# Performance work log

Measured on AMD Instinct MI355X. Metric: run time of the kernel, lower is better.

The kernel has to match this reference:

```python
import jax, jax.numpy as jnp
import numpy as np

K = 40  # neighbors, self.k = 40 in the module
BN_EPS = 1e-5


def knn(x, k):
    # x: (B, C, N) -> indices of k nearest points (largest negative sq-dist)
    xx = jnp.sum(x * x, axis=1, keepdims=True)            # (B, 1, N)
    inner = -2.0 * jnp.einsum('bcn,bcm->bnm', x, x)       # (B, N, N)
    pd = -xx - inner - jnp.swapaxes(xx, 1, 2)             # (B, N, N) = -||xi-xj||^2
    _, idx = jax.lax.top_k(pd, k)                         # (B, N, k)
    return idx


def graph_cov(x, k):
    # Faithful port of get_graph_dynamic_covariance (dim9=False, idx=None)
    B, C, N = x.shape
    idx = knn(x, k)                                       # (B, N, k)
    xt = jnp.swapaxes(x, 1, 2)                            # (B, N, C)
    feature = xt[jnp.arange(B)[:, None, None], idx]       # gather: (B, N, k, C)
    xc = xt[:, :, None, :]                                # (B, N, 1, C)
    rel = feature - xc                                    # relative positions
    var = jnp.var(rel, axis=2, ddof=1)                    # torch.var is unbiased
    relf = rel * (1.0 - var)[:, :, None, :]
    relf = jnp.concatenate([jnp.broadcast_to(xc, rel.shape), relf], axis=3)
    norm = rel - jnp.mean(rel, axis=0)                    # mean over BATCH dim, as in source
    cov = jnp.einsum('bnkc,bnjc->bnkj', rel, norm)        # (B, N, k, k)
    out = jnp.concatenate([relf, cov], axis=3)            # (B, N, k, 2C+k)
    return jnp.transpose(out, (0, 3, 1, 2))               # (B, 2C+k, N, k)


def bn(x, g, b):
    # train-mode BatchNorm (batch statistics, biased variance), eps=1e-5
    axes = (0,) + tuple(range(2, x.ndim))
    m = jnp.mean(x, axis=axes, keepdims=True)
    v = jnp.var(x, axis=axes, keepdims=True)
    shp = (1, -1) + (1,) * (x.ndim - 2)
    return g.reshape(shp) * (x - m) * jax.lax.rsqrt(v + BN_EPS) + b.reshape(shp)


def blk(x, W, g, b):
    # Conv(1x1, no bias) + BN + LeakyReLU(0.2)
    return jax.nn.leaky_relu(bn(jnp.einsum('oi,bi...->bo...', W, x), g, b), 0.2)


def forward(x, l, W3, W4, W5, W6, W7, W8, W9, W10, W11, W12,
            g3, b3, g4, b4, g5, b5, g6, b6, g7, b7, g8, b8, g9, b9,
            g10, b10, g11, b11):
    B, _, N = x.shape
    rc = blk(blk(graph_cov(x, K), W3, g3, b3), W4, g4, b4)       # (B,64,N,K)
    rc_ = jnp.max(rc, axis=-1)                                    # (B,64,N)
    drc = blk(blk(graph_cov(rc_, K), W5, g5, b5), W6, g6, b6)
    drc_ = jnp.max(drc, axis=-1)                                  # (B,64,N)
    allf = jnp.concatenate([rc_, drc_], axis=1)                   # (B,128,N)
    h = jnp.max(blk(allf, W7, g7, b7), axis=-1, keepdims=True)    # (B,1024,1)
    lv = blk(l.reshape(B, -1, 1), W8, g8, b8)                     # (B,64,1)
    h = jnp.concatenate([h, lv], axis=1)                          # (B,1088,1)
    h = jnp.broadcast_to(h, (B, h.shape[1], N))
    h = jnp.concatenate([h, rc_, drc_], axis=1)                   # (B,1216,N)
    h = blk(h, W9, g9, b9)
    h = blk(h, W10, g10, b10)                                     # dropout is eval-mode identity
    h = blk(h, W11, g11, b11)
    return jnp.einsum('oi,bin->bon', W12, h)                      # (B,50,N)


def setup_inputs():
    key = jax.random.key(0)
    ks = jax.random.split(key, 12)
    B, N = 4, 2048
    d = {}
    d['x'] = jax.random.normal(ks[0], (B, 3, N), jnp.float32)
    lab = jax.random.randint(ks[1], (B,), 0, 16)
    d['l'] = jax.nn.one_hot(lab, 16, dtype=jnp.float32)
    wdims = {'W3': (64, 46), 'W4': (64, 64), 'W5': (64, 168), 'W6': (64, 64),
             'W7': (1024, 128), 'W8': (64, 16), 'W9': (512, 1216),
             'W10': (256, 512), 'W11': (128, 256), 'W12': (50, 128)}
    for i, (name, shp) in enumerate(wdims.items()):
        d[name] = jax.random.normal(ks[2 + i], shp, jnp.float32) / np.float32(np.sqrt(shp[1]))
    for name, c in [('g3', 64), ('g4', 64), ('g5', 64), ('g6', 64), ('g7', 1024),
                    ('g8', 64), ('g9', 512), ('g10', 256), ('g11', 128)]:
        d[name] = jnp.ones((c,), jnp.float32)
        d['b' + name[1:]] = jnp.zeros((c,), jnp.float32)
    return d


def reference(x, l, W3, W4, W5, W6, W7, W8, W9, W10, W11, W12,
              g3, b3, g4, b4, g5, b5, g6, b6, g7, b7, g8, b8, g9, b9,
              g10, b10, g11, b11):
    return forward(x, l, W3, W4, W5, W6, W7, W8, W9, W10, W11, W12,
                   g3, b3, g4, b4, g5, b5, g6, b6, g7, b7, g8, b8, g9, b9,
                   g10, b10, g11, b11)
```

## Files before the change

kernel.cpp:

```cpp
#include <hip/hip_runtime.h>
#include <math.h>

#define NB 4
#define NP 2048
#define KNN 40
#define BEPS 1e-5f
#define NSLOT 64
#define CMCH 16

typedef unsigned long long u64;

static __device__ __forceinline__ float leaky(float x) { return x >= 0.f ? x : 0.2f * x; }

static __device__ __forceinline__ u64 keyOf(float v, int m) {
  unsigned u = __float_as_uint(v);
  u ^= (u >> 31) ? 0xFFFFFFFFu : 0x80000000u;
  return ((u64)u << 32) | (unsigned)(NP - 1 - m);
}
static __device__ __forceinline__ u64 umax64(u64 a, u64 b) { return a > b ? a : b; }

__global__ __launch_bounds__(256) void canary_kernel(float* __restrict__ out, int n, float val) {
  int i = blockIdx.x*256 + threadIdx.x;
  if (i < n) out[i] = val;
}

__global__ __launch_bounds__(256) void knn3_kernel(const float* __restrict__ x, int* __restrict__ idx) {
  int b = blockIdx.y, n = blockIdx.x, tid = threadIdx.x;
  __shared__ float pd[NP];
  __shared__ u64 red[256];
  __shared__ u64 red2[32];
  __shared__ int sh_w;
  float xn0 = x[(b*3+0)*NP+n], xn1 = x[(b*3+1)*NP+n], xn2 = x[(b*3+2)*NP+n];
  float xxn = __fadd_rn(__fadd_rn(__fmul_rn(xn0,xn0), __fmul_rn(xn1,xn1)), __fmul_rn(xn2,xn2));
  for (int m = tid; m < NP; m += 256) {
    float m0 = x[(b*3+0)*NP+m], m1 = x[(b*3+1)*NP+m], m2 = x[(b*3+2)*NP+m];
    float xxm = __fadd_rn(__fadd_rn(__fmul_rn(m0,m0), __fmul_rn(m1,m1)), __fmul_rn(m2,m2));
    float dot = __fmaf_rn(xn2, m2, __fmaf_rn(xn1, m1, __fmul_rn(xn0, m0)));
    float inner = __fmul_rn(-2.f, dot);
    pd[m] = __fsub_rn(__fsub_rn(-xxm, inner), xxn);
  }
  __syncthreads();
  u64 myBest = 0;
  #pragma unroll
  for (int j = 0; j < 8; ++j) myBest = umax64(myBest, keyOf(pd[tid + j*256], tid + j*256));
  for (int kk = 0; kk < KNN; ++kk) {
    red[tid] = myBest;
    __syncthreads();
    if (tid < 32) {
      u64 h = red[tid];
      #pragma unroll
      for (int j = 1; j < 8; ++j) h = umax64(h, red[tid + j*32]);
      red2[tid] = h;
    }
    __syncthreads();
    if (tid == 0) {
      u64 h = red2[0];
      #pragma unroll
      for (int j = 1; j < 32; ++j) h = umax64(h, red2[j]);
      int w = NP - 1 - (int)(h & 0xFFFFFFFFu);
      idx[(b*NP+n)*KNN + kk] = w;
      pd[w] = -INFINITY;
      sh_w = w;
    }
    __syncthreads();
    if ((sh_w & 255) == tid) {
      u64 nb = 0;
      #pragma unroll
      for (int j = 0; j < 8; ++j) nb = umax64(nb, keyOf(pd[tid + j*256], tid + j*256));
      myBest = nb;
    }
  }
}

__global__ __launch_bounds__(256) void xx64_kernel(const float* __restrict__ rc, float* __restrict__ xx) {
  int i = blockIdx.x*256 + threadIdx.x;
  if (i >= NB*NP) return;
  const float* p = &rc[(size_t)i*64];
  float s = __fmul_rn(p[0], p[0]);
  #pragma unroll
  for (int c = 1; c < 64; ++c) s = __fadd_rn(s, __fmul_rn(p[c], p[c]));
  xx[i] = s;
}

__global__ __launch_bounds__(256) void knn64_kernel(const float* __restrict__ rc, const float* __restrict__ xx,
                                                    int* __restrict__ idx) {
  int b = blockIdx.y, n = blockIdx.x, tid = threadIdx.x;
  __shared__ float pd[NP];
  __shared__ float xn[64];
  __shared__ u64 red[256];
  __shared__ u64 red2[32];
  __shared__ int sh_w;
  if (tid < 64) xn[tid] = rc[((size_t)b*NP+n)*64 + tid];
  __syncthreads();
  float xxn = xx[b*NP+n];
  for (int m = tid; m < NP; m += 256) {
    const float* xm = &rc[((size_t)b*NP+m)*64];
    float dot = __fmul_rn(xn[0], xm[0]);
    #pragma unroll
    for (int c = 1; c < 64; ++c) dot = __fmaf_rn(xn[c], xm[c], dot);
    float inner = __fmul_rn(-2.f, dot);
    pd[m] = __fsub_rn(__fsub_rn(-xx[b*NP+m], inner), xxn);
  }
  __syncthreads();
  u64 myBest = 0;
  #pragma unroll
  for (int j = 0; j < 8; ++j) myBest = umax64(myBest, keyOf(pd[tid + j*256], tid + j*256));
  for (int kk = 0; kk < KNN; ++kk) {
    red[tid] = myBest;
    __syncthreads();
    if (tid < 32) {
      u64 h = red[tid];
      #pragma unroll
      for (int j = 1; j < 8; ++j) h = umax64(h, red[tid + j*32]);
      red2[tid] = h;
    }
    __syncthreads();
    if (tid == 0) {
      u64 h = red2[0];
      #pragma unroll
      for (int j = 1; j < 32; ++j) h = umax64(h, red2[j]);
      int w = NP - 1 - (int)(h & 0xFFFFFFFFu);
      idx[(b*NP+n)*KNN + kk] = w;
      pd[w] = -INFINITY;
      sh_w = w;
    }
    __syncthreads();
    if ((sh_w & 255) == tid) {
      u64 nb = 0;
      #pragma unroll
      for (int j = 0; j < 8; ++j) nb = umax64(nb, keyOf(pd[tid + j*256], tid + j*256));
      myBest = nb;
    }
  }
}


__global__ __launch_bounds__(256) void s1a_kernel(
    const float* __restrict__ x, const int* __restrict__ idx1, const float* __restrict__ W3,
    double* __restrict__ stslots, float* __restrict__ y)
{
  int b = blockIdx.y, n = blockIdx.x, tid = threadIdx.x;
  __shared__ int sidx[4][KNN];
  __shared__ float rs[KNN][4];
  __shared__ float ns[KNN][4];
  __shared__ float scale[3];
  __shared__ __align__(16) float feat[KNN*48];
  __shared__ float w3s[64*48];
  __shared__ double sred[4][64];

  for (int i = tid; i < 4*KNN; i += 256) sidx[i/KNN][i%KNN] = idx1[((i/KNN)*NP + n)*KNN + (i%KNN)];
  for (int i = tid; i < 64*48; i += 256) { int o = i/48, ci = i%48; w3s[i] = (ci < 46) ? W3[o*46+ci] : 0.f; }
  __syncthreads();
  for (int i = tid; i < KNN*3; i += 256) {
    int k = i/3, c = i%3;
    float ctr = x[(b*3+c)*NP + n];
    float r = x[(b*3+c)*NP + sidx[b][k]] - ctr;
    float s = 0.f;
    for (int b2 = 0; b2 < 4; ++b2) s += x[(b2*3+c)*NP + sidx[b2][k]] - x[(b2*3+c)*NP + n];
    rs[k][c] = r; ns[k][c] = r - 0.25f*s;
  }
  __syncthreads();
  if (tid < 3) {
    float s = 0.f; for (int k = 0; k < KNN; ++k) s += rs[k][tid];
    float m = s/(float)KNN; float v = 0.f;
    for (int k = 0; k < KNN; ++k) { float d = rs[k][tid]-m; v += d*d; }
    scale[tid] = 1.f - v/(float)(KNN-1);
  }
  __syncthreads();
  for (int i = tid; i < KNN*48; i += 256) {
    int k = i/48, ci = i%48; float v;
    if (ci < 3) v = x[(b*3+ci)*NP+n];
    else if (ci < 6) v = rs[k][ci-3]*scale[ci-3];
    else if (ci < 46) { int j = ci-6; v = rs[k][0]*ns[j][0] + rs[k][1]*ns[j][1] + rs[k][2]*ns[j][2]; }
    else v = 0.f;
    feat[i] = v;
  }
  __syncthreads();

  int o = tid & 63, kg = tid >> 6;
  float acc[10];
  #pragma unroll
  for (int t = 0; t < 10; ++t) acc[t] = 0.f;
  for (int ci4 = 0; ci4 < 12; ++ci4) {
    float w0 = w3s[o*48+ci4*4+0], w1 = w3s[o*48+ci4*4+1], w2 = w3s[o*48+ci4*4+2], w3c = w3s[o*48+ci4*4+3];
    #pragma unroll
    for (int t = 0; t < 10; ++t) {
      float4 f4 = *(const float4*)&feat[(kg*10+t)*48 + ci4*4];
      acc[t] += f4.x*w0 + f4.y*w1 + f4.z*w2 + f4.w*w3c;
    }
  }
  size_t bn40 = (size_t)(b*NP+n)*KNN;
  #pragma unroll
  for (int t = 0; t < 10; ++t) y[(bn40 + kg*10+t)*64 + o] = acc[t];
  double s = 0.0, s2 = 0.0;
  #pragma unroll
  for (int t = 0; t < 10; ++t) { double a = acc[t]; s += a; s2 += a*a; }
  int slot = (blockIdx.y*NP + blockIdx.x) & (NSLOT-1);
  sred[kg][o] = s; __syncthreads();
  if (kg == 0) atomicAdd(&stslots[slot*128 + o], sred[0][o]+sred[1][o]+sred[2][o]+sred[3][o]);
  __syncthreads();
  sred[kg][o] = s2; __syncthreads();
  if (kg == 0) atomicAdd(&stslots[slot*128 + 64 + o], sred[0][o]+sred[1][o]+sred[2][o]+sred[3][o]);
}

__global__ __launch_bounds__(256) void s2a_kernel(
    const float* __restrict__ rc, const int* __restrict__ idx2, const float* __restrict__ W5,
    double* __restrict__ stslots, float* __restrict__ y)
{
  int b = blockIdx.y, n = blockIdx.x, tid = threadIdx.x;
  __shared__ int sidx[4][KNN];
  __shared__ float rsT[64*41];
  __shared__ float nsT[64*41];
  __shared__ float scale[64];
  __shared__ __align__(16) float feat[KNN*168];
  __shared__ double sred[4][64];

  for (int i = tid; i < 4*KNN; i += 256) sidx[i/KNN][i%KNN] = idx2[((i/KNN)*NP + n)*KNN + (i%KNN)];
  __syncthreads();
  for (int i = tid; i < KNN*64; i += 256) {
    int k = i >> 6, c = i & 63;
    float ctr = rc[((size_t)(b*NP+n))*64 + c];
    float r = rc[((size_t)(b*NP) + sidx[b][k])*64 + c] - ctr;
    float s = 0.f;
    for (int b2 = 0; b2 < 4; ++b2)
      s += rc[((size_t)(b2*NP) + sidx[b2][k])*64 + c] - rc[((size_t)(b2*NP+n))*64 + c];
    rsT[c*41+k] = r; nsT[c*41+k] = r - 0.25f*s;
  }
  __syncthreads();
  if (tid < 64) {
    int c = tid;
    float s = 0.f; for (int k = 0; k < KNN; ++k) s += rsT[c*41+k];
    float m = s/(float)KNN; float v = 0.f;
    for (int k = 0; k < KNN; ++k) { float d = rsT[c*41+k]-m; v += d*d; }
    scale[c] = 1.f - v/(float)(KNN-1);
  }
  __syncthreads();
  for (int i = tid; i < KNN*128; i += 256) {
    int k = i >> 7, ci = i & 127;
    float v;
    if (ci < 64) v = rc[((size_t)(b*NP+n))*64 + ci];
    else v = rsT[(ci-64)*41 + k]*scale[ci-64];
    feat[k*168 + ci] = v;
  }
  for (int p = tid; p < KNN*KNN; p += 256) {
    int k = p/KNN, j = p%KNN;
    float acc = __fmul_rn(rsT[k], nsT[j]);
    #pragma unroll 8
    for (int c = 1; c < 64; ++c) acc = __fmaf_rn(rsT[c*41+k], nsT[c*41+j], acc);
    feat[k*168 + 128 + j] = acc;
  }
  __syncthreads();

  int o = tid & 63, kg = tid >> 6;
  float acc[10];
  #pragma unroll
  for (int t = 0; t < 10; ++t) acc[t] = 0.f;
  for (int ci4 = 0; ci4 < 42; ++ci4) {
    float4 wv = *(const float4*)&W5[(size_t)o*168 + ci4*4];
    #pragma unroll
    for (int t = 0; t < 10; ++t) {
      float4 f4 = *(const float4*)&feat[(kg*10+t)*168 + ci4*4];
      acc[t] += f4.x*wv.x + f4.y*wv.y + f4.z*wv.z + f4.w*wv.w;
    }
  }
  size_t bn40 = (size_t)(b*NP+n)*KNN;
  #pragma unroll
  for (int t = 0; t < 10; ++t) y[(bn40 + kg*10+t)*64 + o] = acc[t];
  double s = 0.0, s2 = 0.0;
  #pragma unroll
  for (int t = 0; t < 10; ++t) { double a = acc[t]; s += a; s2 += a*a; }
  int slot = (blockIdx.y*NP + blockIdx.x) & (NSLOT-1);
  sred[kg][o] = s; __syncthreads();
  if (kg == 0) atomicAdd(&stslots[slot*128 + o], sred[0][o]+sred[1][o]+sred[2][o]+sred[3][o]);
  __syncthreads();
  sred[kg][o] = s2; __syncthreads();
  if (kg == 0) atomicAdd(&stslots[slot*128 + 64 + o], sred[0][o]+sred[1][o]+sred[2][o]+sred[3][o]);
}

__global__ __launch_bounds__(256) void mid_kernel(
    float* __restrict__ y, const float* __restrict__ W,
    const double* __restrict__ stp, const float* __restrict__ gv, const float* __restrict__ bv,
    double* __restrict__ stslots)
{
  int b = blockIdx.y, n = blockIdx.x, tid = threadIdx.x;
  __shared__ float m_s[64], sc_s[64], bo_s[64];
  __shared__ __align__(16) float ytile[KNN*68];
  __shared__ double sred[4][64];
  const double INV_M1 = 1.0/327680.0;

  if (tid < 64) {
    double md = stp[tid]*INV_M1;
    double vd = stp[64+tid]*INV_M1 - md*md;
    m_s[tid] = (float)md;
    sc_s[tid] = gv[tid]/sqrtf((float)vd + BEPS);
    bo_s[tid] = bv[tid];
  }
  __syncthreads();
  size_t bn40 = (size_t)(b*NP+n)*KNN;
  for (int i = tid; i < KNN*64; i += 256) {
    int k = i >> 6, c = i & 63;
    float v = y[(bn40 + k)*64 + c];
    ytile[k*68+c] = leaky(sc_s[c]*(v - m_s[c]) + bo_s[c]);
  }
  __syncthreads();
  int o = tid & 63, kg = tid >> 6;
  float acc2[10];
  #pragma unroll
  for (int t = 0; t < 10; ++t) acc2[t] = 0.f;
  for (int c4 = 0; c4 < 16; ++c4) {
    float4 wv = *(const float4*)&W[(size_t)o*64 + c4*4];
    #pragma unroll
    for (int t = 0; t < 10; ++t) {
      float4 y4 = *(const float4*)&ytile[(kg*10+t)*68 + c4*4];
      acc2[t] += y4.x*wv.x + y4.y*wv.y + y4.z*wv.z + y4.w*wv.w;
    }
  }
  #pragma unroll
  for (int t = 0; t < 10; ++t) y[(bn40 + kg*10+t)*64 + o] = acc2[t];
  double s = 0.0, s2 = 0.0;
  #pragma unroll
  for (int t = 0; t < 10; ++t) { double a = acc2[t]; s += a; s2 += a*a; }
  int slot = (blockIdx.y*NP + blockIdx.x) & (NSLOT-1);
  sred[kg][o] = s; __syncthreads();
  if (kg == 0) atomicAdd(&stslots[slot*128 + o], sred[0][o]+sred[1][o]+sred[2][o]+sred[3][o]);
  __syncthreads();
  sred[kg][o] = s2; __syncthreads();
  if (kg == 0) atomicAdd(&stslots[slot*128 + 64 + o], sred[0][o]+sred[1][o]+sred[2][o]+sred[3][o]);
}

__global__ __launch_bounds__(256) void maxk_bn_kernel(
    const float* __restrict__ y, const double* __restrict__ stp,
    const float* __restrict__ gv, const float* __restrict__ bv, float* __restrict__ out)
{
  int i = blockIdx.x*256 + threadIdx.x;
  if (i >= NB*NP*64) return;
  int o = i & 63; int bn = i >> 6;
  const double INV_M1 = 1.0/327680.0;
  double md = stp[o]*INV_M1;
  double vd = stp[64+o]*INV_M1 - md*md;
  float m = (float)md;
  float sc = gv[o]/sqrtf((float)vd + BEPS);
  float bo = bv[o];
  float mx = -INFINITY;
  size_t base = (size_t)bn*KNN;
  for (int k = 0; k < KNN; ++k) {
    float v = y[(base + k)*64 + o];
    mx = fmaxf(mx, leaky(sc*(v-m) + bo));
  }
  out[(size_t)bn*64 + o] = mx;
}

__global__ __launch_bounds__(128) void redstats_kernel(const double* __restrict__ slots, double* __restrict__ st) {
  int c = threadIdx.x;
  double s = 0.0;
  for (int i = 0; i < NSLOT; ++i) s += slots[i*128 + c];
  st[c] = s;
}

__global__ __launch_bounds__(256) void allf_kernel(const float* __restrict__ rc, const float* __restrict__ drc,
                                                   float* __restrict__ out) {
  int i = blockIdx.x*256 + threadIdx.x;
  if (i >= NB*NP*128) return;
  int c = i & 127; int bn = i >> 7;
  out[i] = (c < 64) ? rc[(size_t)bn*64 + c] : drc[(size_t)bn*64 + (c-64)];
}

#define GBM 64
#define GBN 64
#define GBK 16
__global__ __launch_bounds__(256) void gemm_kernel(const float* __restrict__ A, const float* __restrict__ W,
                                                   float* __restrict__ C, int M, int No, int Kd,
                                                   int wstride, int woff, const float* __restrict__ bias) {
  __shared__ __align__(16) float As[GBK][GBM+8];
  __shared__ __align__(16) float Ws[GBK][GBN+8];
  int bm = blockIdx.y * GBM, bn = blockIdx.x * GBN;
  int tid = threadIdx.x;
  int tx = tid % 16, ty = tid / 16;
  float acc[4][4] = {{0.f}};
  for (int k0 = 0; k0 < Kd; k0 += GBK) {
    for (int i = tid; i < GBM*GBK; i += 256) {
      int r = i / GBK, c = i % GBK;
      int gm = bm + r, gk = k0 + c;
      As[c][r] = (gk < Kd && gm < M) ? A[(size_t)gm*Kd + gk] : 0.f;
      int gn = bn + r;
      Ws[c][r] = (gk < Kd && gn < No) ? W[(size_t)gn*wstride + woff + gk] : 0.f;
    }
    __syncthreads();
    #pragma unroll
    for (int kk = 0; kk < GBK; ++kk) {
      float4 a4 = *(const float4*)&As[kk][ty*4];
      float4 w4 = *(const float4*)&Ws[kk][tx*4];
      float av[4] = {a4.x, a4.y, a4.z, a4.w};
      float wv[4] = {w4.x, w4.y, w4.z, w4.w};
      #pragma unroll
      for (int i2 = 0; i2 < 4; ++i2)
        #pragma unroll
        for (int j2 = 0; j2 < 4; ++j2)
          acc[i2][j2] += av[i2]*wv[j2];
    }
    __syncthreads();
  }
  for (int i2 = 0; i2 < 4; ++i2) {
    int gm = bm + ty*4 + i2;
    if (gm >= M) continue;
    for (int j2 = 0; j2 < 4; ++j2) {
      int gn = bn + tx*4 + j2;
      if (gn < No) {
        float v = acc[i2][j2];
        if (bias) v += bias[(gm >> 11)*No + gn];
        C[(size_t)gm*No + gn] = v;
      }
    }
  }
}

__global__ __launch_bounds__(256) void colstats_kernel(const float* __restrict__ A, long M, int C,
                                                       int rowsPerBlock, double* __restrict__ st) {
  long r0 = (long)blockIdx.x * rowsPerBlock;
  long r1 = r0 + rowsPerBlock; if (r1 > M) r1 = M;
  int tid = threadIdx.x;
  if (C >= 256) {
    for (int c0 = 0; c0 < C; c0 += 256) {
      int c = c0 + tid;
      double s = 0.0, s2 = 0.0;
      for (long r = r0; r < r1; ++r) { double v = A[r*(long)C + c]; s += v; s2 += v*v; }
      atomicAdd(&st[c], s); atomicAdd(&st[C+c], s2);
    }
  } else {
    int c = tid % C; int grp = tid / C; int G = 256 / C;
    double s = 0.0, s2 = 0.0;
    for (long r = r0 + grp; r < r1; r += G) { double v = A[r*(long)C + c]; s += v; s2 += v*v; }
    __shared__ double sh[512];
    sh[tid] = s; sh[256+tid] = s2; __syncthreads();
    for (int g = G/2; g > 0; g >>= 1) {
      if (grp < g) { sh[tid] += sh[tid + g*C]; sh[256+tid] += sh[256+tid + g*C]; }
      __syncthreads();
    }
    if (grp == 0) { atomicAdd(&st[c], sh[tid]); atomicAdd(&st[C+c], sh[256+tid]); }
  }
}

__global__ __launch_bounds__(256) void bnapply_kernel(float* __restrict__ A, const double* __restrict__ st,
                                                      const float* __restrict__ g, const float* __restrict__ bb,
                                                      double invM, int cmask, size_t total) {
  size_t i = (size_t)blockIdx.x*256 + threadIdx.x;
  if (i >= total) return;
  int c = (int)(i & cmask);
  int C = cmask + 1;
  double md = st[c]*invM;
  double vd = st[C+c]*invM - md*md;
  float m = (float)md;
  float sc = g[c]/sqrtf((float)vd + BEPS);
  float y = sc*(A[i]-m) + bb[c];
  A[i] = leaky(y);
}

__global__ __launch_bounds__(256) void colmax_part_kernel(const float* __restrict__ A, int C,
                                                          float* __restrict__ pmax) {
  int i = blockIdx.x*256 + threadIdx.x;
  if (i >= NB*CMCH*C) return;
  int c = i % C; int t = i / C; int ch = t % CMCH; int b = t / CMCH;
  int n0 = ch * (NP/CMCH);
  float mx = -INFINITY;
  for (int n = n0; n < n0 + NP/CMCH; ++n)
    mx = fmaxf(mx, A[((size_t)(b*NP+n))*C + c]);
  pmax[(size_t)(b*CMCH+ch)*C + c] = mx;
}
__global__ __launch_bounds__(256) void colmax_fin_kernel(const float* __restrict__ pmax, int C,
                                                         float* __restrict__ out) {
  int i = blockIdx.x*256 + threadIdx.x;
  if (i >= NB*C) return;
  int b = i / C, c = i % C;
  float mx = -INFINITY;
  for (int ch = 0; ch < CMCH; ++ch) mx = fmaxf(mx, pmax[(size_t)(b*CMCH+ch)*C + c]);
  out[i] = mx;
}

__global__ __launch_bounds__(256) void lv_kernel(const float* __restrict__ l, const float* __restrict__ W8,
                                                 const float* __restrict__ g8, const float* __restrict__ b8,
                                                 float* __restrict__ lv) {
  __shared__ float raw[4][64];
  int tid = threadIdx.x;
  {
    int b = tid / 64, o = tid % 64;
    float s = 0.f;
    for (int i = 0; i < 16; ++i) s += W8[o*16+i]*l[b*16+i];
    raw[b][o] = s;
  }
  __syncthreads();
  if (tid < 64) {
    int o = tid;
    float m = (raw[0][o]+raw[1][o]+raw[2][o]+raw[3][o])*0.25f;
    float v = 0.f;
    for (int b = 0; b < 4; ++b) { float d = raw[b][o]-m; v += d*d; }
    v *= 0.25f;
    float sc = g8[o]/sqrtf(v + BEPS);
    for (int b = 0; b < 4; ++b) {
      float y = sc*(raw[b][o]-m) + b8[o];
      lv[b*64+o] = leaky(y);
    }
  }
}

__global__ __launch_bounds__(256) void bias9_kernel(const float* __restrict__ hmax, const float* __restrict__ lv,
                                                    const float* __restrict__ W9, float* __restrict__ bias9) {
  int i = blockIdx.x*256 + threadIdx.x;
  if (i >= 4*512) return;
  int b = i >> 9, o = i & 511;
  const float* wr = &W9[(size_t)o*1216];
  float s = 0.f;
  for (int c = 0; c < 1024; ++c) s += hmax[b*1024+c]*wr[c];
  for (int c = 0; c < 64; ++c) s += lv[b*64+c]*wr[1024+c];
  bias9[i] = s;
}

__global__ __launch_bounds__(256) void out_kernel(const float* __restrict__ h5, float* __restrict__ out) {
  int i = blockIdx.x*256 + threadIdx.x;
  if (i >= NB*50*NP) return;
  int n = i % NP; int t = i / NP; int o = t % 50; int b = t / 50;
  out[i] = h5[((size_t)(b*NP+n))*50 + o];
}

extern "C" void kernel_launch(void* const* d_in, const int* in_sizes, int n_in,
                              void* d_out, int out_size, void* d_ws, size_t ws_size,
                              hipStream_t stream) {
  const float* x   = (const float*)d_in[0];
  const float* l   = (const float*)d_in[1];
  const float* W3  = (const float*)d_in[2];
  const float* W4  = (const float*)d_in[3];
  const float* W5  = (const float*)d_in[4];
  const float* W6  = (const float*)d_in[5];
  const float* W7  = (const float*)d_in[6];
  const float* W8  = (const float*)d_in[7];
  const float* W9  = (const float*)d_in[8];
  const float* W10 = (const float*)d_in[9];
  const float* W11 = (const float*)d_in[10];
  const float* W12 = (const float*)d_in[11];
  const float* g3 = (const float*)d_in[12], *b3 = (const float*)d_in[13];
  const float* g4 = (const float*)d_in[14], *b4 = (const float*)d_in[15];
  const float* g5 = (const float*)d_in[16], *b5 = (const float*)d_in[17];
  const float* g6 = (const float*)d_in[18], *b6 = (const float*)d_in[19];
  const float* g7 = (const float*)d_in[20], *b7 = (const float*)d_in[21];
  const float* g8 = (const float*)d_in[22], *b8 = (const float*)d_in[23];
  const float* g9 = (const float*)d_in[24], *b9 = (const float*)d_in[25];
  const float* g10 = (const float*)d_in[26], *b10 = (const float*)d_in[27];
  const float* g11 = (const float*)d_in[28], *b11 = (const float*)d_in[29];
  (void)in_sizes; (void)n_in;

  constexpr size_t OFF_IDX1 = 0;
  constexpr size_t OFF_IDX2 = OFF_IDX1 + (size_t)NB*NP*KNN*4;
  constexpr size_t OFF_RC   = OFF_IDX2 + (size_t)NB*NP*KNN*4;
  constexpr size_t OFF_DRC  = OFF_RC   + (size_t)NB*NP*64*4;
  constexpr size_t OFF_XX   = OFF_DRC  + (size_t)NB*NP*64*4;
  constexpr size_t OFF_SLOT = OFF_XX   + (size_t)NB*NP*4;
  constexpr size_t OFF_ST3  = OFF_SLOT + (size_t)NSLOT*128*8;
  constexpr size_t OFF_ST4  = OFF_ST3 + 128*8;
  constexpr size_t OFF_ST5  = OFF_ST4 + 128*8;
  constexpr size_t OFF_ST6  = OFF_ST5 + 128*8;
  constexpr size_t OFF_STH  = OFF_ST6 + 128*8;
  constexpr size_t OFF_HMAX = OFF_STH + 2*1024*8;
  constexpr size_t OFF_LV   = OFF_HMAX + 4*1024*4;
  constexpr size_t OFF_B9   = OFF_LV + 4096;
  constexpr size_t OFF_PMAX = OFF_B9 + 4*512*4;
  constexpr size_t OFF_ALLF = OFF_PMAX + (size_t)NB*CMCH*1024*4;
  constexpr size_t OFF_H1   = OFF_ALLF + (size_t)NB*NP*128*4;
  constexpr size_t SZ_H1    = (size_t)NB*NP*1024*4;
  constexpr size_t OFF_END  = OFF_H1 + SZ_H1;
  constexpr size_t OFF_H2 = OFF_H1;
  constexpr size_t OFF_H3 = OFF_H2 + (size_t)NB*NP*512*4;
  constexpr size_t OFF_H4 = OFF_H3 + (size_t)NB*NP*256*4;
  constexpr size_t OFF_H5 = OFF_H4 + (size_t)NB*NP*128*4;
  static_assert(OFF_H5 + (size_t)NB*NP*50*4 <= OFF_END, "h alias overflow");
  constexpr size_t OFF_Y   = OFF_END;
  constexpr size_t SZ_Y    = (size_t)NB*NP*KNN*64*4;
  constexpr size_t OFF_FAST_END = OFF_Y + SZ_Y;

  if (ws_size < OFF_END) {
    canary_kernel<<<(out_size + 255)/256, 256, 0, stream>>>((float*)d_out, out_size, (float)(ws_size >> 20));
    return;
  }
  const bool FAST = (ws_size >= OFF_FAST_END);

  char* ws = (char*)d_ws;
  int*    idx1  = (int*)(ws + OFF_IDX1);
  int*    idx2  = (int*)(ws + OFF_IDX2);
  float*  rc    = (float*)(ws + OFF_RC);
  float*  drc   = (float*)(ws + OFF_DRC);
  float*  xx2   = (float*)(ws + OFF_XX);
  double* slots = (double*)(ws + OFF_SLOT);
  double* st3s  = (double*)(ws + OFF_ST3);
  double* st4s  = (double*)(ws + OFF_ST4);
  double* st5s  = (double*)(ws + OFF_ST5);
  double* st6s  = (double*)(ws + OFF_ST6);
  double* sth   = (double*)(ws + OFF_STH);
  float*  hmaxb = (float*)(ws + OFF_HMAX);
  float*  lvb   = (float*)(ws + OFF_LV);
  float*  bias9 = (float*)(ws + OFF_B9);
  float*  pmaxb = (float*)(ws + OFF_PMAX);
  float*  allf  = (float*)(ws + OFF_ALLF);
  float*  h1    = (float*)(ws + OFF_H1);
  float*  h2    = (float*)(ws + OFF_H2);
  float*  h3    = (float*)(ws + OFF_H3);
  float*  h4    = (float*)(ws + OFF_H4);
  float*  h5    = (float*)(ws + OFF_H5);
  float*  ybuf  = (float*)(ws + OFF_Y);

  dim3 gridNP(NP, NB);
  const size_t slotBytes = (size_t)NSLOT*128*8;
  const double INV_M2 = 1.0/8192.0;

  knn3_kernel<<<gridNP, 256, 0, stream>>>(x, idx1);
  hipMemsetAsync(slots, 0, slotBytes, stream);
  s1a_kernel<<<gridNP, 256, 0, stream>>>(x, idx1, W3, slots, FAST ? ybuf : h1);
  redstats_kernel<<<1, 128, 0, stream>>>(slots, st3s);
  hipMemsetAsync(slots, 0, slotBytes, stream);
  mid_kernel<<<gridNP, 256, 0, stream>>>(FAST ? ybuf : h1, W4, st3s, g3, b3, slots);
  redstats_kernel<<<1, 128, 0, stream>>>(slots, st4s);
  maxk_bn_kernel<<<(NB*NP*64 + 255)/256, 256, 0, stream>>>(FAST ? ybuf : h1, st4s, g4, b4, rc);

  xx64_kernel<<<(NB*NP + 255)/256, 256, 0, stream>>>(rc, xx2);
  knn64_kernel<<<gridNP, 256, 0, stream>>>(rc, xx2, idx2);
  hipMemsetAsync(slots, 0, slotBytes, stream);
  s2a_kernel<<<gridNP, 256, 0, stream>>>(rc, idx2, W5, slots, FAST ? ybuf : h1);
  redstats_kernel<<<1, 128, 0, stream>>>(slots, st5s);
  hipMemsetAsync(slots, 0, slotBytes, stream);
  mid_kernel<<<gridNP, 256, 0, stream>>>(FAST ? ybuf : h1, W6, st5s, g5, b5, slots);
  redstats_kernel<<<1, 128, 0, stream>>>(slots, st6s);
  maxk_bn_kernel<<<(NB*NP*64 + 255)/256, 256, 0, stream>>>(FAST ? ybuf : h1, st6s, g6, b6, drc);

  allf_kernel<<<(NB*NP*128 + 255)/256, 256, 0, stream>>>(rc, drc, allf);
  gemm_kernel<<<dim3(1024/GBN, 8192/GBM), 256, 0, stream>>>(allf, W7, h1, 8192, 1024, 128, 128, 0, nullptr);
  hipMemsetAsync(sth, 0, 2*1024*8, stream);
  colstats_kernel<<<128, 256, 0, stream>>>(h1, 8192, 1024, 64, sth);
  bnapply_kernel<<<(unsigned)(((size_t)8192*1024 + 255)/256), 256, 0, stream>>>(h1, sth, g7, b7, INV_M2, 1023, (size_t)8192*1024);
  colmax_part_kernel<<<(NB*CMCH*1024 + 255)/256, 256, 0, stream>>>(h1, 1024, pmaxb);
  colmax_fin_kernel<<<(NB*1024 + 255)/256, 256, 0, stream>>>(pmaxb, 1024, hmaxb);
  lv_kernel<<<1, 256, 0, stream>>>(l, W8, g8, b8, lvb);
  bias9_kernel<<<8, 256, 0, stream>>>(hmaxb, lvb, W9, bias9);

  gemm_kernel<<<dim3(512/GBN, 8192/GBM), 256, 0, stream>>>(allf, W9, h2, 8192, 512, 128, 1216, 1088, bias9);
  hipMemsetAsync(sth, 0, 2*512*8, stream);
  colstats_kernel<<<128, 256, 0, stream>>>(h2, 8192, 512, 64, sth);
  bnapply_kernel<<<(unsigned)(((size_t)8192*512 + 255)/256), 256, 0, stream>>>(h2, sth, g9, b9, INV_M2, 511, (size_t)8192*512);

  gemm_kernel<<<dim3(256/GBN, 8192/GBM), 256, 0, stream>>>(h2, W10, h3, 8192, 256, 512, 512, 0, nullptr);
  hipMemsetAsync(sth, 0, 2*256*8, stream);
  colstats_kernel<<<128, 256, 0, stream>>>(h3, 8192, 256, 64, sth);
  bnapply_kernel<<<(unsigned)(((size_t)8192*256 + 255)/256), 256, 0, stream>>>(h3, sth, g10, b10, INV_M2, 255, (size_t)8192*256);

  gemm_kernel<<<dim3(128/GBN, 8192/GBM), 256, 0, stream>>>(h3, W11, h4, 8192, 128, 256, 256, 0, nullptr);
  hipMemsetAsync(sth, 0, 2*128*8, stream);
  colstats_kernel<<<128, 256, 0, stream>>>(h4, 8192, 128, 64, sth);
  bnapply_kernel<<<(unsigned)(((size_t)8192*128 + 255)/256), 256, 0, stream>>>(h4, sth, g11, b11, INV_M2, 127, (size_t)8192*128);

  gemm_kernel<<<dim3(1, 8192/GBM), 256, 0, stream>>>(h4, W12, h5, 8192, 50, 128, 128, 0, nullptr);
  out_kernel<<<(NB*50*NP + 255)/256, 256, 0, stream>>>(h5, (float*)d_out);
}
```

Measured before the change: 1.788 ms.

## Replace block-wide top-k reduction with per-wavefront shuffle top-k and merge

The k-NN selection over 64-dim features drops the three-barrier shared-memory argmax per neighbor. Each of four wavefronts now independently extracts its own top-40 from a 512-point slice using register-held keys and xor-shuffle max reductions. A single thread then merges the four sorted lists. This removes 120 block barriers per query point, at the cost of redundant per-wave selection work and a serial merge on one thread.

Measured after the change: 1.785 ms. No clear change (-0.1%).

```diff
diff --git a/kernel.cpp b/kernel.cpp
--- a/kernel.cpp
+++ b/kernel.cpp
@@ -87,9 +87,7 @@
   int b = blockIdx.y, n = blockIdx.x, tid = threadIdx.x;
   __shared__ float pd[NP];
   __shared__ float xn[64];
-  __shared__ u64 red[256];
-  __shared__ u64 red2[32];
-  __shared__ int sh_w;
+  __shared__ u64 locKey[4*KNN];
   if (tid < 64) xn[tid] = rc[((size_t)b*NP+n)*64 + tid];
   __syncthreads();
   float xxn = xx[b*NP+n];
@@ -102,34 +100,55 @@
     pd[m] = __fsub_rn(__fsub_rn(-xx[b*NP+m], inner), xxn);
   }
   __syncthreads();
-  u64 myBest = 0;
-  #pragma unroll
-  for (int j = 0; j < 8; ++j) myBest = umax64(myBest, keyOf(pd[tid + j*256], tid + j*256));
+
+  int lane = tid & 63, wid = tid >> 6;
+  int base = wid*512 + lane;
+  u64 kq0 = keyOf(pd[base + 0*64], base + 0*64);
+  u64 kq1 = keyOf(pd[base + 1*64], base + 1*64);
+  u64 kq2 = keyOf(pd[base + 2*64], base + 2*64);
+  u64 kq3 = keyOf(pd[base + 3*64], base + 3*64);
+  u64 kq4 = keyOf(pd[base + 4*64], base + 4*64);
+  u64 kq5 = keyOf(pd[base + 5*64], base + 5*64);
+  u64 kq6 = keyOf(pd[base + 6*64], base + 6*64);
+  u64 kq7 = keyOf(pd[base + 7*64], base + 7*64);
+  unsigned alive = 0xFFu;
+  u64 hl = umax64(umax64(umax64(kq0,kq1), umax64(kq2,kq3)), umax64(umax64(kq4,kq5), umax64(kq6,kq7)));
   for (int kk = 0; kk < KNN; ++kk) {
-    red[tid] = myBest;
-    __syncthreads();
-    if (tid < 32) {
-      u64 h = red[tid];
-      #pragma unroll
-      for (int j = 1; j < 8; ++j) h = umax64(h, red[tid + j*32]);
-      red2[tid] = h;
-    }
-    __syncthreads();
-    if (tid == 0) {
-      u64 h = red2[0];
-      #pragma unroll
-      for (int j = 1; j < 32; ++j) h = umax64(h, red2[j]);
-      int w = NP - 1 - (int)(h & 0xFFFFFFFFu);
-      idx[(b*NP+n)*KNN + kk] = w;
-      pd[w] = -INFINITY;
-      sh_w = w;
-    }
-    __syncthreads();
-    if ((sh_w & 255) == tid) {
-      u64 nb = 0;
-      #pragma unroll
-      for (int j = 0; j < 8; ++j) nb = umax64(nb, keyOf(pd[tid + j*256], tid + j*256));
-      myBest = nb;
+    u64 h = hl;
+    #pragma unroll
+    for (int off = 32; off >= 1; off >>= 1)
+      h = umax64(h, (u64)__shfl_xor((unsigned long long)h, off, 64));
+    int m = NP - 1 - (int)(h & 0xFFFFFFFFu);
+    if (lane == (m & 63)) {
+      alive &= ~(1u << ((m >> 6) & 7));
+      u64 nh = 0;
+      if (alive & 1u)   nh = umax64(nh, kq0);
+      if (alive & 2u)   nh = umax64(nh, kq1);
+      if (alive & 4u)   nh = umax64(nh, kq2);
+      if (alive & 8u)   nh = umax64(nh, kq3);
+      if (alive & 16u)  nh = umax64(nh, kq4);
+      if (alive & 32u)  nh = umax64(nh, kq5);
+      if (alive & 64u)  nh = umax64(nh, kq6);
+      if (alive & 128u) nh = umax64(nh, kq7);
+      hl = nh;
+    }
+    if (lane == 0) locKey[wid*KNN + kk] = h;
+  }
+  __syncthreads();
+  if (tid == 0) {
+    int p0 = 0, p1 = 0, p2 = 0, p3 = 0;
+    int* outp = &idx[(b*NP+n)*KNN];
+    for (int kk = 0; kk < KNN; ++kk) {
+      u64 c0 = (p0 < KNN) ? locKey[0*KNN + p0] : 0;
+      u64 c1 = (p1 < KNN) ? locKey[1*KNN + p1] : 0;
+      u64 c2 = (p2 < KNN) ? locKey[2*KNN + p2] : 0;
+      u64 c3 = (p3 < KNN) ? locKey[3*KNN + p3] : 0;
+      u64 best = umax64(umax64(c0, c1), umax64(c2, c3));
+      if (best == c0) ++p0;
+      else if (best == c1) ++p1;
+      else if (best == c2) ++p2;
+      else ++p3;
+      outp[kk] = NP - 1 - (int)(best & 0xFFFFFFFFu);
     }
   }
 }
```
